# Kernel tuning notes

Measured on AMD Instinct MI355X. Metric: run time of the kernel, lower is better.

Reference implementation:

```python
import jax, jax.numpy as jnp
import numpy as np

B, T, V, D, H, C = 256, 512, 400000, 50, 50, 5  # batch, seq, vocab, emb_dim, lstm_hidden, classes


def setup_inputs() -> dict:
    key = jax.random.key(0)
    ks = jax.random.split(key, 9)
    x = jax.random.randint(ks[0], (B, T), 0, V)
    lengths = jax.random.randint(ks[1], (B,), 1, T + 1)
    bows = jnp.zeros((B, 1), dtype=jnp.float32)  # unused by the model
    emb_table = jax.random.normal(ks[2], (V, D), dtype=jnp.float32) * 0.1
    s = 1.0 / np.sqrt(H)
    W_ih = jax.random.uniform(ks[3], (4 * H, D), minval=-s, maxval=s, dtype=jnp.float32)
    W_hh = jax.random.uniform(ks[4], (4 * H, H), minval=-s, maxval=s, dtype=jnp.float32)
    b_ih = jax.random.uniform(ks[5], (4 * H,), minval=-s, maxval=s, dtype=jnp.float32)
    b_hh = jax.random.uniform(ks[6], (4 * H,), minval=-s, maxval=s, dtype=jnp.float32)
    sl = 1.0 / np.sqrt(3 * H)
    W_lin = jax.random.uniform(ks[7], (C, 3 * H), minval=-sl, maxval=sl, dtype=jnp.float32)
    b_lin = jax.random.uniform(ks[8], (C,), minval=-sl, maxval=sl, dtype=jnp.float32)
    return {"x": x, "lengths": lengths, "bows": bows, "emb_table": emb_table,
            "W_ih": W_ih, "W_hh": W_hh, "b_ih": b_ih, "b_hh": b_hh,
            "W_lin": W_lin, "b_lin": b_lin}


def _lstm(emb, W_ih, W_hh, b_ih, b_hh):
    # emb: [B,T,D] -> h_all: [B,T,H]; PyTorch gate order i,f,g,o
    xp = jnp.einsum('btd,gd->btg', emb, W_ih) + b_ih + b_hh  # [B,T,4H]
    xp_t = jnp.swapaxes(xp, 0, 1)  # [T,B,4H]
    h0 = jnp.zeros((emb.shape[0], W_hh.shape[1]), emb.dtype)
    c0 = jnp.zeros_like(h0)

    def step(carry, xt):
        h, c = carry
        g = xt + h @ W_hh.T
        i, f, gg, o = jnp.split(g, 4, axis=-1)
        i, f, o = jax.nn.sigmoid(i), jax.nn.sigmoid(f), jax.nn.sigmoid(o)
        c = f * c + i * jnp.tanh(gg)
        h = o * jnp.tanh(c)
        return (h, c), h

    _, h_all = jax.lax.scan(step, (h0, c0), xp_t)
    return jnp.swapaxes(h_all, 0, 1)  # [B,T,H]


def reference(x, lengths, bows, emb_table, W_ih, W_hh, b_ih, b_hh, W_lin, b_lin):
    emb = emb_table[x]                              # [B,T,D]
    h_all = _lstm(emb, W_ih, W_hh, b_ih, b_hh)      # [B,T,H]
    idx = jnp.minimum(lengths, h_all.shape[1]) - 1  # last valid timestep
    last = jnp.take_along_axis(h_all, idx[:, None, None], axis=1)[:, 0, :]  # [B,H]
    # faithful to original: sum over full padded seq / length, max over full padded seq
    mean = jnp.sum(emb, axis=1) / lengths[:, None].astype(emb.dtype)        # [B,D]
    mx = jnp.max(emb, axis=1)                                               # [B,D]
    rep = jnp.concatenate([last, mean, mx], axis=1)                          # [B,3H]
    return rep @ W_lin.T + b_lin
```

## Files before the change

### kernel.cpp

```cpp
#include <hip/hip_runtime.h>
#include <cmath>

#define NB 256
#define NT 512
#define ND 50
#define NH 50
#define NC 5

typedef float f32x4 __attribute__((ext_vector_type(4)));

__device__ __forceinline__ float rcpf(float x) { return __builtin_amdgcn_rcpf(x); }

template<int CTRL>
__device__ __forceinline__ float qp(float x) {
    int xi = __float_as_int(x);
    return __int_as_float(__builtin_amdgcn_update_dpp(xi, xi, CTRL, 0xF, 0xF, false));
}
__device__ __forceinline__ float swz4(float x) {
    return __int_as_float(__builtin_amdgcn_ds_swizzle(__float_as_int(x), 0x101F));
}

__device__ __forceinline__ void gload4(f32x4& d, const float* p) {
    asm volatile("global_load_dwordx4 %0, %1, off" : "=v"(d) : "v"(p));
}
__device__ __forceinline__ void gload1(float& d, const float* p) {
    asm volatile("global_load_dword %0, %1, off" : "=v"(d) : "v"(p));
}

__global__ __launch_bounds__(256)
void k0_prep(const float* __restrict__ W_hh, const float* __restrict__ W_ih,
             float* __restrict__ wsWih, float* __restrict__ wsWhh2)
{
    int idx = blockIdx.x * 256 + threadIdx.x;
    if (idx < 200 * 52) {
        int d = idx / 52, c = idx - (idx / 52) * 52;
        wsWih[idx] = (c < ND) ? W_ih[d * ND + c] : 0.f;
    } else if (idx < 200 * 52 + 400 * 28) {
        int j0 = idx - 200 * 52;
        int lane = j0 / 28, j = j0 - (j0 / 28) * 28;
        int k = lane >> 3, h_ = (lane >> 2) & 1, q = lane & 3;
        int r = q * NH + k;
        float v = 0.f;
        if (j < 24)       v = W_hh[r * NH + 2 * j + h_];
        else if (j == 24) v = W_hh[r * NH + 48 + h_];
        wsWhh2[j0] = v;
    }
}

#define LOADW13(wrow) f32x4 w0{},w1{},w2{},w3{},w4{},w5{},w6{},w7{},w8{},w9{},w10{},w11{},w12{}; \
    gload4(w0,(wrow)+0); gload4(w1,(wrow)+4); gload4(w2,(wrow)+8); gload4(w3,(wrow)+12); \
    gload4(w4,(wrow)+16); gload4(w5,(wrow)+20); gload4(w6,(wrow)+24); gload4(w7,(wrow)+28); \
    gload4(w8,(wrow)+32); gload4(w9,(wrow)+36); gload4(w10,(wrow)+40); gload4(w11,(wrow)+44); \
    gload4(w12,(wrow)+48);

#define DOT(J, HP) { f32x4 h4 = (HP)[J];                          \
    a0 = fmaf(h4.x, w##J.x, a0); a1 = fmaf(h4.y, w##J.y, a1);     \
    a2 = fmaf(h4.z, w##J.z, a2); a3 = fmaf(h4.w, w##J.w, a3); }
#define DOT13(HP) DOT(0,HP) DOT(1,HP) DOT(2,HP) DOT(3,HP) DOT(4,HP) DOT(5,HP) \
    DOT(6,HP) DOT(7,HP) DOT(8,HP) DOT(9,HP) DOT(10,HP) DOT(11,HP) DOT(12,HP)

__global__ __launch_bounds__(256)
void k1_xproj(const int* __restrict__ x, const int* __restrict__ lengths,
              const float* __restrict__ emb_table,
              const float* __restrict__ wsWih, const float* __restrict__ b_ih,
              const float* __restrict__ b_hh,
              float* __restrict__ xp, int t0, int t1, int tiles, int tcAlloc)
{
    const int b    = blockIdx.x / tiles;
    const int tile = blockIdx.x % tiles;
    const int rt0  = t0 + tile * 64;
    if (rt0 >= t1) return;
    if (rt0 >= lengths[b]) return;
    const int nrows = min(64, t1 - rt0);

    __shared__ int xv[64];
    __shared__ __align__(16) float eL[64][52];

    const int tid = threadIdx.x;

    float bsum = 0.f;
    const float* wrow = wsWih + tid * 52;
    LOADW13(wrow)
    if (tid < 200) bsum = b_ih[tid] + b_hh[tid];
    if (tid < nrows) xv[tid] = x[(size_t)b * NT + rt0 + tid];
    __syncthreads();
    for (int idx = tid; idx < nrows * 52; idx += 256) {
        int row = idx / 52, col = idx - row * 52;
        eL[row][col] = (col < ND) ? emb_table[(size_t)xv[row] * ND + col] : 0.f;
    }
    asm volatile("s_waitcnt vmcnt(0)" ::: "memory");
    __builtin_amdgcn_sched_barrier(0);
    __syncthreads();
    if (tid < 200) {
        const int wr = 4 * (tid % NH) + (tid / NH);
        float* xpb = xp + ((size_t)b * tcAlloc + (rt0 - t0)) * 200 + wr;
        for (int row = 0; row < nrows; ++row) {
            const f32x4* ep = (const f32x4*)&eL[row][0];
            float a0 = bsum, a1 = 0.f, a2 = 0.f, a3 = 0.f;
            DOT13(ep)
            xpb[(size_t)row * 200] = (a0 + a1) + (a2 + a3);
        }
    }
}

#define FENCE_BAR                                             \
    asm volatile("s_waitcnt lgkmcnt(0)" ::: "memory");        \
    __builtin_amdgcn_s_barrier();                             \
    asm volatile("" ::: "memory");

__global__ __launch_bounds__(512, 1)
void k2_scan(const int* __restrict__ lengths, const float* __restrict__ wsWhh2,
             const float* __restrict__ xp,
             float* __restrict__ stH, float* __restrict__ stC, float* __restrict__ lastH,
             int t0, int t1, int tcAlloc)
{
    const int b = blockIdx.x, tid = threadIdx.x;
    __shared__ __align__(16) float hbX[2][2][28];
    __shared__ __align__(16) float ring[4][256];

    const bool gm = tid < 400;
    const bool st = tid >= 448;
    const int  k  = tid >> 3;
    const int  h_ = (tid >> 2) & 1;
    const int  q  = tid & 3;
    const bool b0v = q & 1, b1v = q & 2;
    const int  nsteps = t1 - t0;

    int lastidx = min(lengths[b], NT) - 1;
    float cst = 0.f;
    if (gm) cst = (t0 == 0) ? 0.f : stC[b * NH + k];
    if (tid < NH) hbX[0][tid & 1][tid >> 1] = (t0 == 0) ? 0.f : stH[b * NH + tid];

    f32x4 P0{}, P1{}, P2{}, P3{}, P4{}, P5{}; float wtail = 0.f;
    float scale = 1.f, addc = 0.f, hkeep = 0.f, hfin = 0.f;
    if (gm) {
        const float* wr_ = wsWhh2 + tid * 28;
        gload4(P0, wr_ + 0);  gload4(P1, wr_ + 4);  gload4(P2, wr_ + 8);
        gload4(P3, wr_ + 12); gload4(P4, wr_ + 16); gload4(P5, wr_ + 20);
        gload1(wtail, wr_ + 24);
        asm volatile("s_waitcnt vmcnt(0)" ::: "memory");
        if (q == 2) { scale = 2.f; addc = -1.f; }
    }

    const float* xpb = xp + (size_t)b * tcAlloc * 200;
    const int sl = tid - 448;
    f32x4 p1{}, p2{}, p3{};
    if (st) {
        f32x4 p0 = *(const f32x4*)(xpb + 0 * 200 + 4 * sl);
        p1 = *(const f32x4*)(xpb + 1 * 200 + 4 * sl);
        p2 = *(const f32x4*)(xpb + 2 * 200 + 4 * sl);
        p3 = *(const f32x4*)(xpb + 3 * 200 + 4 * sl);
        *(f32x4*)&ring[0][4 * sl] = p0;
    }
    FENCE_BAR

    for (int s = 0; s < nsteps; ++s) {
        if (gm) {
            const float* hp = &hbX[s & 1][h_][0];
            const f32x4* hq = (const f32x4*)hp;
            f32x4 h0 = hq[0], h1 = hq[1], h2 = hq[2], h3 = hq[3], h4 = hq[4], h5 = hq[5];
            float htail = hp[24];
            float xq = ring[s & 3][(k << 2) | q];
            float acc0 = h_ ? 0.f : xq;
            float acc1 = 0.f;
            acc0 = fmaf(h0.x, P0.x, acc0); acc1 = fmaf(h0.y, P0.y, acc1);
            acc0 = fmaf(h0.z, P0.z, acc0); acc1 = fmaf(h0.w, P0.w, acc1);
            acc0 = fmaf(h1.x, P1.x, acc0); acc1 = fmaf(h1.y, P1.y, acc1);
            acc0 = fmaf(h1.z, P1.z, acc0); acc1 = fmaf(h1.w, P1.w, acc1);
            acc0 = fmaf(h2.x, P2.x, acc0); acc1 = fmaf(h2.y, P2.y, acc1);
            acc0 = fmaf(h2.z, P2.z, acc0); acc1 = fmaf(h2.w, P2.w, acc1);
            acc0 = fmaf(h3.x, P3.x, acc0); acc1 = fmaf(h3.y, P3.y, acc1);
            acc0 = fmaf(h3.z, P3.z, acc0); acc1 = fmaf(h3.w, P3.w, acc1);
            acc0 = fmaf(h4.x, P4.x, acc0); acc1 = fmaf(h4.y, P4.y, acc1);
            acc0 = fmaf(h4.z, P4.z, acc0); acc1 = fmaf(h4.w, P4.w, acc1);
            acc0 = fmaf(h5.x, P5.x, acc0); acc1 = fmaf(h5.y, P5.y, acc1);
            acc0 = fmaf(h5.z, P5.z, acc0); acc1 = fmaf(h5.w, P5.w, acc1);
            acc1 = fmaf(htail, wtail, acc1);
            float u = acc0 + swz4(acc0);
            float v = acc1 + swz4(acc1);
            float g = u + v;
            float act = fmaf(rcpf(1.f + __expf(-scale * g)), scale, addc);
            float v1 = qp<0xB1>(act);
            float v2 = qp<0x4E>(act);
            float v3 = qp<0x4E>(v1);
            float i_  = b1v ? (b0v ? v3 : v2) : (b0v ? v1 : act);
            float f_  = b1v ? (b0v ? v2 : v3) : (b0v ? act : v1);
            float gt_ = b1v ? (b0v ? v1 : act) : (b0v ? v3 : v2);
            float o_  = b1v ? (b0v ? act : v1) : (b0v ? v2 : v3);
            cst = fmaf(f_, cst, i_ * gt_);
            float th = fmaf(rcpf(1.f + __expf(-2.f * cst)), 2.f, -1.f);
            float hv = o_ * th;
            if ((tid & 7) == 0) hbX[(s & 1) ^ 1][k & 1][k >> 1] = hv;
            hfin = hv;
            hkeep = (t0 + s == lastidx) ? hv : hkeep;
        }
        if (st) {
            *(f32x4*)&ring[(s + 1) & 3][4 * sl] = p1;
            f32x4 pn = *(const f32x4*)(xpb + (size_t)(s + 4) * 200 + 4 * sl);
            p1 = p2; p2 = p3; p3 = pn;
        }
        FENCE_BAR
    }

    if (gm && (tid & 7) == 0) {
        stH[b * NH + k] = hfin;
        stC[b * NH + k] = cst;
        if (lastidx >= t0 && lastidx < t1) lastH[b * NH + k] = hkeep;
    }
}

__global__ __launch_bounds__(256)
void k3_final(const int* __restrict__ x, const int* __restrict__ lengths,
              const float* __restrict__ emb_table,
              const float* __restrict__ W_lin, const float* __restrict__ b_lin,
              const float* __restrict__ lastH, float* __restrict__ out)
{
    const int b = blockIdx.x, tid = threadIdx.x;
    __shared__ int xv[NT];
    __shared__ float ps[5][52], pm[5][52];
    __shared__ float rep[160];

    for (int i = tid; i < NT; i += 256) xv[i] = x[(size_t)b * NT + i];
    __syncthreads();
    const int g = tid / ND, d = tid - g * ND;
    if (tid < 250) {
        float s = 0.f, m = -INFINITY;
        #pragma unroll 4
        for (int t = g; t < NT; t += 5) {
            float e = emb_table[(size_t)xv[t] * ND + d];
            s += e; m = fmaxf(m, e);
        }
        ps[g][d] = s; pm[g][d] = m;
    }
    __syncthreads();
    if (tid < NH) {
        float s = ps[0][tid] + ps[1][tid] + ps[2][tid] + ps[3][tid] + ps[4][tid];
        float m = fmaxf(fmaxf(fmaxf(pm[0][tid], pm[1][tid]), fmaxf(pm[2][tid], pm[3][tid])), pm[4][tid]);
        rep[tid]          = lastH[b * NH + tid];
        rep[NH + tid]     = s / (float)lengths[b];
        rep[2 * NH + tid] = m;
    }
    __syncthreads();
    if (tid < NC) {
        float acc = b_lin[tid];
        #pragma unroll 5
        for (int j = 0; j < 3 * NH; ++j)
            acc = fmaf(rep[j], W_lin[tid * 3 * NH + j], acc);
        out[(size_t)b * NC + tid] = acc;
    }
}

extern "C" void kernel_launch(void* const* d_in, const int* in_sizes, int n_in,
                              void* d_out, int out_size, void* d_ws, size_t ws_size,
                              hipStream_t stream) {
    const int*   x     = (const int*)d_in[0];
    const int*   len   = (const int*)d_in[1];
    const float* emb   = (const float*)d_in[3];
    const float* W_ih  = (const float*)d_in[4];
    const float* W_hh  = (const float*)d_in[5];
    const float* b_ih  = (const float*)d_in[6];
    const float* b_hh  = (const float*)d_in[7];
    const float* W_lin = (const float*)d_in[8];
    const float* b_lin = (const float*)d_in[9];
    float* outp = (float*)d_out;

    float* stH    = (float*)d_ws;
    float* stC    = stH + NB * NH;
    float* lastH  = stC + NB * NH;
    float* wsWih  = (float*)((char*)d_ws + 160 * 1024);
    float* wsWhh2 = wsWih + 200 * 52;
    const size_t xpOff = 256 * 1024;
    float* xp = (float*)((char*)d_ws + xpOff);

    size_t avail = (ws_size > xpOff + 8192) ? ws_size - xpOff - 8192 : 0;
    int tc = (int)(avail / ((size_t)NB * 200 * sizeof(float)));
    tc &= ~3;
    if (tc > NT) tc = NT;
    if (tc < 4)  tc = 4;

    hipLaunchKernelGGL(k0_prep, dim3(85), dim3(256), 0, stream, W_hh, W_ih, wsWih, wsWhh2);

    for (int t0 = 0; t0 < NT; t0 += tc) {
        const int t1 = min(NT, t0 + tc);
        const int tiles = (t1 - t0 + 63) / 64;
        hipLaunchKernelGGL(k1_xproj, dim3(NB * tiles), dim3(256), 0, stream,
                           x, len, emb, wsWih, b_ih, b_hh, xp, t0, t1, tiles, tc);
        hipLaunchKernelGGL(k2_scan, dim3(NB), dim3(512), 0, stream,
                           len, wsWhh2, xp, stH, stC, lastH, t0, t1, tc);
    }
    hipLaunchKernelGGL(k3_final, dim3(NB), dim3(256), 0, stream,
                       x, len, emb, W_lin, b_lin, lastH, outp);
}
```

Measured before the change: 310.9 us.

## Repartition LSTM recurrent matvec so each lane computes two gates over a quarter of h

The recurrent step is remapped. Each group of 8 lanes per hidden unit used to split the 50-wide h vector in halves across 4 gate lanes. Now each lane covers a quarter of h (13 elements) and accumulates two gates, with reductions done by two DPP quad-permute steps and gate exchange by one swizzle. The W_hh prep layout and the h shared buffer (now 4 strided slices, zero-padded) change to match. The aim is fewer LDS reads per lane per step and a shorter select tree on the serial critical path, at the cost of an extra reduction stage and two exps computed per lane.

After: 308.6 us. No clear change (-0.7%).

```diff
diff --git a/kernel.cpp b/kernel.cpp
--- a/kernel.cpp
+++ b/kernel.cpp
@@ -8,6 +8,7 @@
 #define NC 5
 
 typedef float f32x4 __attribute__((ext_vector_type(4)));
+typedef float f32x2 __attribute__((ext_vector_type(2)));
 
 __device__ __forceinline__ float rcpf(float x) { return __builtin_amdgcn_rcpf(x); }
 
@@ -23,13 +24,13 @@
 __device__ __forceinline__ void gload4(f32x4& d, const float* p) {
     asm volatile("global_load_dwordx4 %0, %1, off" : "=v"(d) : "v"(p));
 }
-__device__ __forceinline__ void gload1(float& d, const float* p) {
-    asm volatile("global_load_dword %0, %1, off" : "=v"(d) : "v"(p));
+__device__ __forceinline__ void gload2(f32x2& d, const float* p) {
+    asm volatile("global_load_dwordx2 %0, %1, off" : "=v"(d) : "v"(p));
 }
 
 __global__ __launch_bounds__(256)
 void k0_prep(const float* __restrict__ W_hh, const float* __restrict__ W_ih,
-             float* __restrict__ wsWih, float* __restrict__ wsWhh2)
+             float* __restrict__ wsWih, float* __restrict__ wsW2)
 {
     int idx = blockIdx.x * 256 + threadIdx.x;
     if (idx < 200 * 52) {
@@ -37,27 +38,28 @@
         wsWih[idx] = (c < ND) ? W_ih[d * ND + c] : 0.f;
     } else if (idx < 200 * 52 + 400 * 28) {
         int j0 = idx - 200 * 52;
-        int lane = j0 / 28, j = j0 - (j0 / 28) * 28;
-        int k = lane >> 3, h_ = (lane >> 2) & 1, q = lane & 3;
-        int r = q * NH + k;
+        int lane = j0 / 28, w = j0 - (j0 / 28) * 28;
+        int k = lane >> 3, h2 = (lane >> 2) & 1, p = lane & 3;
         float v = 0.f;
-        if (j < 24)       v = W_hh[r * NH + 2 * j + h_];
-        else if (j == 24) v = W_hh[r * NH + 48 + h_];
-        wsWhh2[j0] = v;
-    }
-}
-
-#define LOADW13(wrow) f32x4 w0{},w1{},w2{},w3{},w4{},w5{},w6{},w7{},w8{},w9{},w10{},w11{},w12{}; \
-    gload4(w0,(wrow)+0); gload4(w1,(wrow)+4); gload4(w2,(wrow)+8); gload4(w3,(wrow)+12); \
-    gload4(w4,(wrow)+16); gload4(w5,(wrow)+20); gload4(w6,(wrow)+24); gload4(w7,(wrow)+28); \
-    gload4(w8,(wrow)+32); gload4(w9,(wrow)+36); gload4(w10,(wrow)+40); gload4(w11,(wrow)+44); \
-    gload4(w12,(wrow)+48);
-
-#define DOT(J, HP) { f32x4 h4 = (HP)[J];                          \
+        if (w < 24) {
+            int m = w >> 1, gb = w & 1;
+            int gate = 2 * h2 + gb;
+            int j = 4 * m + p;
+            v = W_hh[(gate * NH + k) * NH + j];
+        } else if (w == 24 || w == 25) {
+            int gate = 2 * h2 + (w - 24);
+            if (p == 2)      v = W_hh[(gate * NH + k) * NH + 48];
+            else if (p == 3) v = W_hh[(gate * NH + k) * NH + 49];
+        }
+        wsW2[j0] = v;
+    }
+}
+
+#define DOTI(J, HP) { f32x4 h4 = (HP)[J];                          \
     a0 = fmaf(h4.x, w##J.x, a0); a1 = fmaf(h4.y, w##J.y, a1);     \
     a2 = fmaf(h4.z, w##J.z, a2); a3 = fmaf(h4.w, w##J.w, a3); }
-#define DOT13(HP) DOT(0,HP) DOT(1,HP) DOT(2,HP) DOT(3,HP) DOT(4,HP) DOT(5,HP) \
-    DOT(6,HP) DOT(7,HP) DOT(8,HP) DOT(9,HP) DOT(10,HP) DOT(11,HP) DOT(12,HP)
+#define DOTI13(HP) DOTI(0,HP) DOTI(1,HP) DOTI(2,HP) DOTI(3,HP) DOTI(4,HP) DOTI(5,HP) \
+    DOTI(6,HP) DOTI(7,HP) DOTI(8,HP) DOTI(9,HP) DOTI(10,HP) DOTI(11,HP) DOTI(12,HP)
 
 __global__ __launch_bounds__(256)
 void k1_xproj(const int* __restrict__ x, const int* __restrict__ lengths,
@@ -80,7 +82,11 @@
 
     float bsum = 0.f;
     const float* wrow = wsWih + tid * 52;
-    LOADW13(wrow)
+    f32x4 w0{},w1{},w2{},w3{},w4{},w5{},w6{},w7{},w8{},w9{},w10{},w11{},w12{};
+    gload4(w0,wrow+0); gload4(w1,wrow+4); gload4(w2,wrow+8); gload4(w3,wrow+12);
+    gload4(w4,wrow+16); gload4(w5,wrow+20); gload4(w6,wrow+24); gload4(w7,wrow+28);
+    gload4(w8,wrow+32); gload4(w9,wrow+36); gload4(w10,wrow+40); gload4(w11,wrow+44);
+    gload4(w12,wrow+48);
     if (tid < 200) bsum = b_ih[tid] + b_hh[tid];
     if (tid < nrows) xv[tid] = x[(size_t)b * NT + rt0 + tid];
     __syncthreads();
@@ -97,7 +103,7 @@
         for (int row = 0; row < nrows; ++row) {
             const f32x4* ep = (const f32x4*)&eL[row][0];
             float a0 = bsum, a1 = 0.f, a2 = 0.f, a3 = 0.f;
-            DOT13(ep)
+            DOTI13(ep)
             xpb[(size_t)row * 200] = (a0 + a1) + (a2 + a3);
         }
     }
@@ -109,88 +115,93 @@
     asm volatile("" ::: "memory");
 
 __global__ __launch_bounds__(512, 1)
-void k2_scan(const int* __restrict__ lengths, const float* __restrict__ wsWhh2,
+void k2_scan(const int* __restrict__ lengths, const float* __restrict__ wsW2,
              const float* __restrict__ xp,
              float* __restrict__ stH, float* __restrict__ stC, float* __restrict__ lastH,
              int t0, int t1, int tcAlloc)
 {
     const int b = blockIdx.x, tid = threadIdx.x;
-    __shared__ __align__(16) float hbX[2][2][28];
+    __shared__ __align__(16) float hT[2][4][36];
     __shared__ __align__(16) float ring[4][256];
 
-    const bool gm = tid < 400;
-    const bool st = tid >= 448;
-    const int  k  = tid >> 3;
-    const int  h_ = (tid >> 2) & 1;
-    const int  q  = tid & 3;
-    const bool b0v = q & 1, b1v = q & 2;
+    const bool gm   = tid < 400;
+    const bool st   = tid >= 448;
+    const int  k    = tid >> 3;
+    const int  h_   = (tid >> 2) & 1;
+    const int  p    = tid & 3;
+    const bool isp0 = (p == 0);
+    const bool h1v  = (h_ == 1);
+    const bool wlead = gm && ((tid & 7) == 0);
     const int  nsteps = t1 - t0;
 
     int lastidx = min(lengths[b], NT) - 1;
-    float cst = 0.f;
-    if (gm) cst = (t0 == 0) ? 0.f : stC[b * NH + k];
-    if (tid < NH) hbX[0][tid & 1][tid >> 1] = (t0 == 0) ? 0.f : stH[b * NH + tid];
-
-    f32x4 P0{}, P1{}, P2{}, P3{}, P4{}, P5{}; float wtail = 0.f;
-    float scale = 1.f, addc = 0.f, hkeep = 0.f, hfin = 0.f;
+    float cst = 0.f, hinit = 0.f;
+    if (gm && t0 != 0) cst = stC[b * NH + k];
+    if (tid < NH && t0 != 0) hinit = stH[b * NH + tid];
+    if (tid < 288) ((float*)hT)[tid] = 0.f;
+    __syncthreads();
+    if (tid < NH) hT[0][tid & 3][tid >> 2] = hinit;
+
+    f32x4 A0{}, A1{}, A2{}, A3{}, A4{}, A5{};
+    f32x2 T{};
+    float sce = 1.f, ade = 0.f, hkeep = 0.f, hfin = 0.f;
     if (gm) {
-        const float* wr_ = wsWhh2 + tid * 28;
-        gload4(P0, wr_ + 0);  gload4(P1, wr_ + 4);  gload4(P2, wr_ + 8);
-        gload4(P3, wr_ + 12); gload4(P4, wr_ + 16); gload4(P5, wr_ + 20);
-        gload1(wtail, wr_ + 24);
+        const float* wr_ = wsW2 + tid * 28;
+        gload4(A0, wr_ + 0);  gload4(A1, wr_ + 4);  gload4(A2, wr_ + 8);
+        gload4(A3, wr_ + 12); gload4(A4, wr_ + 16); gload4(A5, wr_ + 20);
+        gload2(T, wr_ + 24);
         asm volatile("s_waitcnt vmcnt(0)" ::: "memory");
-        if (q == 2) { scale = 2.f; addc = -1.f; }
-    }
-
+        __builtin_amdgcn_sched_barrier(0);
+        if (h1v) { sce = 2.f; ade = -1.f; }
+    }
     const float* xpb = xp + (size_t)b * tcAlloc * 200;
     const int sl = tid - 448;
     f32x4 p1{}, p2{}, p3{};
     if (st) {
-        f32x4 p0 = *(const f32x4*)(xpb + 0 * 200 + 4 * sl);
+        f32x4 q0 = *(const f32x4*)(xpb + 0 * 200 + 4 * sl);
         p1 = *(const f32x4*)(xpb + 1 * 200 + 4 * sl);
         p2 = *(const f32x4*)(xpb + 2 * 200 + 4 * sl);
         p3 = *(const f32x4*)(xpb + 3 * 200 + 4 * sl);
-        *(f32x4*)&ring[0][4 * sl] = p0;
+        *(f32x4*)&ring[0][4 * sl] = q0;
     }
     FENCE_BAR
 
     for (int s = 0; s < nsteps; ++s) {
         if (gm) {
-            const float* hp = &hbX[s & 1][h_][0];
+            const int cur = s & 1;
+            const float* hp = &hT[cur][p][0];
             const f32x4* hq = (const f32x4*)hp;
-            f32x4 h0 = hq[0], h1 = hq[1], h2 = hq[2], h3 = hq[3], h4 = hq[4], h5 = hq[5];
-            float htail = hp[24];
-            float xq = ring[s & 3][(k << 2) | q];
-            float acc0 = h_ ? 0.f : xq;
-            float acc1 = 0.f;
-            acc0 = fmaf(h0.x, P0.x, acc0); acc1 = fmaf(h0.y, P0.y, acc1);
-            acc0 = fmaf(h0.z, P0.z, acc0); acc1 = fmaf(h0.w, P0.w, acc1);
-            acc0 = fmaf(h1.x, P1.x, acc0); acc1 = fmaf(h1.y, P1.y, acc1);
-            acc0 = fmaf(h1.z, P1.z, acc0); acc1 = fmaf(h1.w, P1.w, acc1);
-            acc0 = fmaf(h2.x, P2.x, acc0); acc1 = fmaf(h2.y, P2.y, acc1);
-            acc0 = fmaf(h2.z, P2.z, acc0); acc1 = fmaf(h2.w, P2.w, acc1);
-            acc0 = fmaf(h3.x, P3.x, acc0); acc1 = fmaf(h3.y, P3.y, acc1);
-            acc0 = fmaf(h3.z, P3.z, acc0); acc1 = fmaf(h3.w, P3.w, acc1);
-            acc0 = fmaf(h4.x, P4.x, acc0); acc1 = fmaf(h4.y, P4.y, acc1);
-            acc0 = fmaf(h4.z, P4.z, acc0); acc1 = fmaf(h4.w, P4.w, acc1);
-            acc0 = fmaf(h5.x, P5.x, acc0); acc1 = fmaf(h5.y, P5.y, acc1);
-            acc0 = fmaf(h5.z, P5.z, acc0); acc1 = fmaf(h5.w, P5.w, acc1);
-            acc1 = fmaf(htail, wtail, acc1);
-            float u = acc0 + swz4(acc0);
-            float v = acc1 + swz4(acc1);
-            float g = u + v;
-            float act = fmaf(rcpf(1.f + __expf(-scale * g)), scale, addc);
-            float v1 = qp<0xB1>(act);
-            float v2 = qp<0x4E>(act);
-            float v3 = qp<0x4E>(v1);
-            float i_  = b1v ? (b0v ? v3 : v2) : (b0v ? v1 : act);
-            float f_  = b1v ? (b0v ? v2 : v3) : (b0v ? act : v1);
-            float gt_ = b1v ? (b0v ? v1 : act) : (b0v ? v3 : v2);
-            float o_  = b1v ? (b0v ? act : v1) : (b0v ? v2 : v3);
-            cst = fmaf(f_, cst, i_ * gt_);
+            f32x4 h0 = hq[0], h1 = hq[1], h2 = hq[2];
+            float htl = hT[cur][p ^ 2][12];
+            f32x2 xq = *(const f32x2*)&ring[s & 3][(k << 2) | (h_ << 1)];
+            float ae = isp0 ? xq.x : 0.f;
+            float ao = isp0 ? xq.y : 0.f;
+            ae = fmaf(h0.x, A0.x, ae); ao = fmaf(h0.x, A0.y, ao);
+            ae = fmaf(h0.y, A0.z, ae); ao = fmaf(h0.y, A0.w, ao);
+            ae = fmaf(h0.z, A1.x, ae); ao = fmaf(h0.z, A1.y, ao);
+            ae = fmaf(h0.w, A1.z, ae); ao = fmaf(h0.w, A1.w, ao);
+            ae = fmaf(h1.x, A2.x, ae); ao = fmaf(h1.x, A2.y, ao);
+            ae = fmaf(h1.y, A2.z, ae); ao = fmaf(h1.y, A2.w, ao);
+            ae = fmaf(h1.z, A3.x, ae); ao = fmaf(h1.z, A3.y, ao);
+            ae = fmaf(h1.w, A3.z, ae); ao = fmaf(h1.w, A3.w, ao);
+            ae = fmaf(h2.x, A4.x, ae); ao = fmaf(h2.x, A4.y, ao);
+            ae = fmaf(h2.y, A4.z, ae); ao = fmaf(h2.y, A4.w, ao);
+            ae = fmaf(h2.z, A5.x, ae); ao = fmaf(h2.z, A5.y, ao);
+            ae = fmaf(h2.w, A5.z, ae); ao = fmaf(h2.w, A5.w, ao);
+            ae = fmaf(htl, T.x, ae);   ao = fmaf(htl, T.y, ao);
+            float te = ae + qp<0xB1>(ae); te = te + qp<0x4E>(te);
+            float to = ao + qp<0xB1>(ao); to = to + qp<0x4E>(to);
+            float acte = fmaf(rcpf(1.f + __expf(-sce * te)), sce, ade);
+            float acto = rcpf(1.f + __expf(-to));
+            float oe = swz4(acte), oo = swz4(acto);
+            float i_ = h1v ? oe : acte;
+            float f_ = h1v ? oo : acto;
+            float g_ = h1v ? acte : oe;
+            float o_ = h1v ? acto : oo;
+            cst = fmaf(f_, cst, i_ * g_);
             float th = fmaf(rcpf(1.f + __expf(-2.f * cst)), 2.f, -1.f);
             float hv = o_ * th;
-            if ((tid & 7) == 0) hbX[(s & 1) ^ 1][k & 1][k >> 1] = hv;
+            if (wlead) hT[cur ^ 1][k & 3][k >> 2] = hv;
             hfin = hv;
             hkeep = (t0 + s == lastidx) ? hv : hkeep;
         }
@@ -202,7 +213,7 @@
         FENCE_BAR
     }
 
-    if (gm && (tid & 7) == 0) {
+    if (wlead) {
         stH[b * NH + k] = hfin;
         stC[b * NH + k] = cst;
         if (lastidx >= t0 && lastidx < t1) lastH[b * NH + k] = hkeep;
@@ -264,11 +275,11 @@
     const float* b_lin = (const float*)d_in[9];
     float* outp = (float*)d_out;
 
-    float* stH    = (float*)d_ws;
-    float* stC    = stH + NB * NH;
-    float* lastH  = stC + NB * NH;
-    float* wsWih  = (float*)((char*)d_ws + 160 * 1024);
-    float* wsWhh2 = wsWih + 200 * 52;
+    float* stH   = (float*)d_ws;
+    float* stC   = stH + NB * NH;
+    float* lastH = stC + NB * NH;
+    float* wsWih = (float*)((char*)d_ws + 160 * 1024);
+    float* wsW2  = wsWih + 200 * 52;
     const size_t xpOff = 256 * 1024;
     float* xp = (float*)((char*)d_ws + xpOff);
 
@@ -278,7 +289,7 @@
     if (tc > NT) tc = NT;
     if (tc < 4)  tc = 4;
 
-    hipLaunchKernelGGL(k0_prep, dim3(85), dim3(256), 0, stream, W_hh, W_ih, wsWih, wsWhh2);
+    hipLaunchKernelGGL(k0_prep, dim3(85), dim3(256), 0, stream, W_hh, W_ih, wsWih, wsW2);
 
     for (int t0 = 0; t0 < NT; t0 += tc) {
         const int t1 = min(NT, t0 + tc);
@@ -286,7 +297,7 @@
         hipLaunchKernelGGL(k1_xproj, dim3(NB * tiles), dim3(256), 0, stream,
                            x, len, emb, wsWih, b_ih, b_hh, xp, t0, t1, tiles, tc);
         hipLaunchKernelGGL(k2_scan, dim3(NB), dim3(512), 0, stream,
-                           len, wsWhh2, xp, stH, stC, lastH, t0, t1, tc);
+                           len, wsW2, xp, stH, stC, lastH, t0, t1, tc);
     }
     hipLaunchKernelGGL(k3_final, dim3(NB), dim3(256), 0, stream,
                        x, len, emb, W_lin, b_lin, lastH, outp);
```
